# Performance work log

Measured on AMD Instinct MI355X. Metric: run time of the kernel, lower is better.

The kernel has to match this reference:

```python
import jax, jax.numpy as jnp
import numpy as np

B, C, EMB, W, H = 4, 128, 16, 64, 64


def setup_inputs() -> dict:
    key = jax.random.key(0)
    ks = jax.random.split(key, 8)
    return {
        "x": jax.random.normal(ks[0], (B, C, W, H), dtype=jnp.float32),
        "Wq": jax.random.normal(ks[1], (EMB, C), dtype=jnp.float32) * (1.0 / np.sqrt(C)),
        "bq": jax.random.normal(ks[2], (EMB,), dtype=jnp.float32) * 0.01,
        "Wk": jax.random.normal(ks[3], (EMB, C), dtype=jnp.float32) * (1.0 / np.sqrt(C)),
        "bk": jax.random.normal(ks[4], (EMB,), dtype=jnp.float32) * 0.01,
        "Wv": jax.random.normal(ks[5], (C, C), dtype=jnp.float32) * (1.0 / np.sqrt(C)),
        "bv": jax.random.normal(ks[6], (C,), dtype=jnp.float32) * 0.01,
        "gamma": jax.random.normal(ks[7], (1,), dtype=jnp.float32),
    }


def reference(x, Wq, bq, Wk, bk, Wv, bv, gamma):
    b, c, w, h = x.shape
    n = w * h
    xf = x.reshape(b, c, n)  # flatten spatial: [b, c, n]
    # 1x1 convs == per-pixel linear maps
    q = jnp.einsum('ec,bcn->bne', Wq, xf) + bq                # [b, n, emb]
    k = jnp.einsum('ec,bcn->ben', Wk, xf) + bk[:, None]       # [b, emb, n]
    energy = jnp.einsum('bne,bem->bnm', q, k)                 # [b, n, n] (unscaled)
    attn = jax.nn.softmax(energy, axis=-1)                    # softmax over keys m
    v = jnp.einsum('dc,bcn->bdn', Wv, xf) + bv[:, None]       # [b, c, n]
    # torch: out = bmm(V, attn^T) -> out[b,d,n] = sum_m V[b,d,m] * attn[b,n,m]
    out = jnp.einsum('bdm,bnm->bdn', v, attn)
    out = (gamma * out + xf).reshape(b, c, w, h)
    return out
```

## Files before the change

kernel.cpp:

```cpp
#include <hip/hip_runtime.h>


#define PEXP(s) exp2f(fmaf((s), 1.44269504f, -23.08312065f))

typedef __attribute__((ext_vector_type(8))) short bf16x8;
typedef __attribute__((ext_vector_type(4))) float f32x4;
typedef __attribute__((ext_vector_type(4))) int i32x4;

__device__ __forceinline__ bf16x8 asbf(i32x4 v) {
  return __builtin_bit_cast(bf16x8, v);
}
__device__ __forceinline__ int cvtpk(float lo, float hi) {
  int r;
  asm("v_cvt_pk_bf16_f32 %0, %1, %2" : "=v"(r) : "v"(lo), "v"(hi));
  return r;
}
__device__ __forceinline__ float lo16f(int u) {
  return __uint_as_float(((unsigned)u) << 16);
}
__device__ __forceinline__ float hi16f(int u) {
  return __uint_as_float(((unsigned)u) & 0xffff0000u);
}
__device__ __forceinline__ void async16(const void* g, void* l) {
  __builtin_amdgcn_global_load_lds(
      (const __attribute__((address_space(1))) void*)g,
      (__attribute__((address_space(3))) void*)l, 16, 0, 0);
}


__global__ __launch_bounds__(256, 2) void proj_kernel(
    const float* __restrict__ xg, const float* __restrict__ Wq,
    const float* __restrict__ bq, const float* __restrict__ Wk,
    const float* __restrict__ bk, const float* __restrict__ Wv,
    const float* __restrict__ bv, char* __restrict__ Qg,
    char* __restrict__ Kg, char* __restrict__ Vg) {
  __shared__ __align__(16) float xl[8192];
  __shared__ __align__(16) float wl[10240];
  const int bid = blockIdx.x;
  const int xcd = bid & 7, b = xcd >> 1, dh = xcd & 1, pt = bid >> 3;
  const int n0 = pt << 6;
  const int tid = threadIdx.x;

  const float* Wqk = dh ? Wk : Wq;
#pragma unroll
  for (int k = 0; k < 8; k++) {
    int idx = tid + k * 256;
    int cc = idx >> 4, p4 = (idx & 15) << 2;
    const float* src = xg + ((size_t)(b * 128 + cc)) * 4096 + n0 + p4;
    async16(src, (char*)xl + idx * 16);
  }
#pragma unroll
  for (int k = 0; k < 10; k++) {
    int j = tid + k * 256;
    int row = j >> 5, c4 = (j & 31) * 4;
    const float* src = (k < 8) ? (Wv + (size_t)(dh * 64 + row) * 128 + c4)
                               : (Wqk + (size_t)(row - 64) * 128 + c4);
    async16(src, (char*)wl + j * 16);
  }
  asm volatile("s_waitcnt vmcnt(0)" ::: "memory");
  __syncthreads();

  const int px = tid & 63, og = tid >> 6;

  float av[16];
#pragma unroll
  for (int i = 0; i < 16; i++) av[i] = 0.f;
  float aq[4] = {0.f, 0.f, 0.f, 0.f};

  for (int c0 = 0; c0 < 128; c0 += 4) {
    float x0 = xl[(c0 + 0) * 64 + px];
    float x1 = xl[(c0 + 1) * 64 + px];
    float x2 = xl[(c0 + 2) * 64 + px];
    float x3 = xl[(c0 + 3) * 64 + px];
#pragma unroll
    for (int r = 0; r < 16; r++) {
      const float* wr = &wl[(og * 16 + r) * 128 + c0];
      av[r] += wr[0] * x0 + wr[1] * x1 + wr[2] * x2 + wr[3] * x3;
    }
#pragma unroll
    for (int ee = 0; ee < 4; ee++) {
      const float* wr = &wl[(64 + og * 4 + ee) * 128 + c0];
      aq[ee] += wr[0] * x0 + wr[1] * x1 + wr[2] * x2 + wr[3] * x3;
    }
  }

  {
    const float* bqk = dh ? bk : bq;
    float v0 = aq[0] + bqk[og * 4 + 0], v1 = aq[1] + bqk[og * 4 + 1];
    float v2 = aq[2] + bqk[og * 4 + 2], v3 = aq[3] + bqk[og * 4 + 3];
    int h0 = cvtpk(v0, v1), h1 = cvtpk(v2, v3);
    float r0 = v0 - lo16f(h0), r1 = v1 - hi16f(h0);
    float r2 = v2 - lo16f(h1), r3 = v3 - hi16f(h1);
    int l0 = cvtpk(r0, r1), l1 = cvtpk(r2, r3);
    i32x4 ch = {h0, h1, l0, l1};
    char* QKg = dh ? Kg : Qg;
    *(i32x4*)(QKg + ((size_t)(b * 16384 + og * 4096 + n0 + px)) * 16) = ch;
  }

  const int d0 = dh * 64 + og * 16;
  __syncthreads();
#pragma unroll
  for (int r = 0; r < 16; r++) xl[(og * 16 + r) * 64 + px] = av[r] + bv[d0 + r];
  __syncthreads();

  char* vg_t = Vg + (size_t)b * 2097152 + (size_t)pt * 32768;
#pragma unroll
  for (int k = 0; k < 4; k++) {
    int id = tid + k * 256;
    int gs = id & 3, d1 = (id >> 2) & 63, kc = id >> 8;
    int d = dh * 64 + d1;
    int gg = gs ^ ((d >> 1) & 3);
    f32x4 v = *(const f32x4*)&xl[d1 * 64 + kc * 16 + gg * 4];
    int h0 = cvtpk(v[0], v[1]), h1 = cvtpk(v[2], v[3]);
    float r0 = v[0] - lo16f(h0), r1 = v[1] - hi16f(h0);
    float r2 = v[2] - lo16f(h1), r3 = v[3] - hi16f(h1);
    int l0 = cvtpk(r0, r1), l1 = cvtpk(r2, r3);
    i32x4 ch = {h0, h1, l0, l1};
    *(i32x4*)(vg_t + ((size_t)((kc * 128 + d) * 4 + gs)) * 16) = ch;
  }
}

#define COMPUTE(KF, V0, V1, V2, V3)                                            \
  {                                                                            \
    i32x4 k2 = {KF[2], KF[3], KF[0], KF[1]};                                   \
    __builtin_amdgcn_s_setprio(1);                                             \
    f32x4 s0 = __builtin_amdgcn_mfma_f32_16x16x32_bf16(asbf(KF), asbf(qf0),    \
                                                       zero4, 0, 0, 0);        \
    s0 = __builtin_amdgcn_mfma_f32_16x16x32_bf16(asbf(k2), asbf(qf0), s0, 0,   \
                                                 0, 0);                        \
    f32x4 s1 = __builtin_amdgcn_mfma_f32_16x16x32_bf16(asbf(KF), asbf(qf1),    \
                                                       zero4, 0, 0, 0);        \
    s1 = __builtin_amdgcn_mfma_f32_16x16x32_bf16(asbf(k2), asbf(qf1), s1, 0,   \
                                                 0, 0);                        \
    __builtin_amdgcn_s_setprio(0);                                             \
    bf16x8 a0, a1;                                                             \
    {                                                                          \
      float p0 = PEXP(s0[0]), p1 = PEXP(s0[1]), p2 = PEXP(s0[2]),              \
            p3 = PEXP(s0[3]);                                                  \
      lsum0 += (p0 + p1) + (p2 + p3);                                          \
      int h0 = cvtpk(p0, p1), h1 = cvtpk(p2, p3);                              \
      i32x4 A = {h0, h1, h0, h1};                                              \
      a0 = asbf(A);                                                            \
    }                                                                          \
    {                                                                          \
      float p0 = PEXP(s1[0]), p1 = PEXP(s1[1]), p2 = PEXP(s1[2]),              \
            p3 = PEXP(s1[3]);                                                  \
      lsum1 += (p0 + p1) + (p2 + p3);                                          \
      int h0 = cvtpk(p0, p1), h1 = cvtpk(p2, p3);                              \
      i32x4 A = {h0, h1, h0, h1};                                              \
      a1 = asbf(A);                                                            \
    }                                                                          \
    __builtin_amdgcn_s_setprio(1);                                             \
    acc[0][0] = __builtin_amdgcn_mfma_f32_16x16x32_bf16(a0, asbf(V0),          \
                                                        acc[0][0], 0, 0, 0);   \
    acc[0][1] = __builtin_amdgcn_mfma_f32_16x16x32_bf16(a0, asbf(V1),          \
                                                        acc[0][1], 0, 0, 0);   \
    acc[0][2] = __builtin_amdgcn_mfma_f32_16x16x32_bf16(a0, asbf(V2),          \
                                                        acc[0][2], 0, 0, 0);   \
    acc[0][3] = __builtin_amdgcn_mfma_f32_16x16x32_bf16(a0, asbf(V3),          \
                                                        acc[0][3], 0, 0, 0);   \
    acc[1][0] = __builtin_amdgcn_mfma_f32_16x16x32_bf16(a1, asbf(V0),          \
                                                        acc[1][0], 0, 0, 0);   \
    acc[1][1] = __builtin_amdgcn_mfma_f32_16x16x32_bf16(a1, asbf(V1),          \
                                                        acc[1][1], 0, 0, 0);   \
    acc[1][2] = __builtin_amdgcn_mfma_f32_16x16x32_bf16(a1, asbf(V2),          \
                                                        acc[1][2], 0, 0, 0);   \
    acc[1][3] = __builtin_amdgcn_mfma_f32_16x16x32_bf16(a1, asbf(V3),          \
                                                        acc[1][3], 0, 0, 0);   \
    __builtin_amdgcn_s_setprio(0);                                             \
  }

#define LOADSET(KF, V0, V1, V2, V3, tt)                                        \
  {                                                                            \
    const char* vp = vlane + (size_t)(tt)*32768;                               \
    V0 = *(const i32x4*)(vp);                                                  \
    V1 = *(const i32x4*)(vp + 1024);                                           \
    V2 = *(const i32x4*)(vp + 2048);                                           \
    V3 = *(const i32x4*)(vp + 3072);                                           \
    KF = *(const i32x4*)(kg_b + ((size_t)(g * 4096 + (tt)*64 + krow)) * 16);   \
  }

__global__ __launch_bounds__(512, 4) void flash_kernel(
    const char* __restrict__ Qg, const char* __restrict__ Kg,
    const char* __restrict__ Vg, const float* __restrict__ xg,
    const float* __restrict__ gammag, float* __restrict__ outg) {
  __shared__ float red_O[32 * 129];
  __shared__ float red_L[32];

  const int bid = blockIdx.x;
  const int xcd = bid & 7;
  const int b = xcd >> 1;
  const int nt = ((bid >> 3) << 1) | (xcd & 1);
  const int n0 = nt << 5;

  const int tid = threadIdx.x;
  const int l = tid & 63, w = tid >> 6;
  const int c = l & 15, g = l >> 4;
  const int kc = w & 3, dh = w >> 2;

  const char* kg_b = Kg + (size_t)b * 262144;
  const char* vg_b = Vg + (size_t)b * 2097152;
  const char* vlane =
      vg_b + ((size_t)(kc * 512 + dh * 256 + c * 4 + (g ^ ((c >> 1) & 3)))) * 16;
  const int krow = kc * 16 + c;

  const i32x4 qf0 =
      *(const i32x4*)(Qg + ((size_t)(b * 16384 + g * 4096 + n0 + c)) * 16);
  const i32x4 qf1 =
      *(const i32x4*)(Qg + ((size_t)(b * 16384 + g * 4096 + n0 + 16 + c)) * 16);

  const f32x4 zero4 = {0.f, 0.f, 0.f, 0.f};
  f32x4 acc[2][4];
#pragma unroll
  for (int qt = 0; qt < 2; qt++)
#pragma unroll
    for (int dt = 0; dt < 4; dt++) acc[qt][dt] = zero4;
  float lsum0 = 0.f, lsum1 = 0.f;

  i32x4 ka, va0, va1, va2, va3;
  i32x4 kb, vb0, vb1, vb2, vb3;
  LOADSET(ka, va0, va1, va2, va3, 0);
  LOADSET(kb, vb0, vb1, vb2, vb3, 1);

  for (int t = 0; t < 64; t += 2) {
    COMPUTE(ka, va0, va1, va2, va3);
    {
      int t2 = (t + 2 < 64) ? t + 2 : 63;
      LOADSET(ka, va0, va1, va2, va3, t2);
    }
    COMPUTE(kb, vb0, vb1, vb2, vb3);
    {
      int t3 = (t + 3 < 64) ? t + 3 : 63;
      LOADSET(kb, vb0, vb1, vb2, vb3, t3);
    }
  }

  for (int i = tid; i < 32 * 129; i += 512) red_O[i] = 0.f;
  if (tid < 32) red_L[tid] = 0.f;
  __syncthreads();

  {
    float s = lsum0;
    s += __shfl_xor(s, 16);
    s += __shfl_xor(s, 32);
    if (g == 0 && dh == 0) atomicAdd(&red_L[c], s);
    s = lsum1;
    s += __shfl_xor(s, 16);
    s += __shfl_xor(s, 32);
    if (g == 0 && dh == 0) atomicAdd(&red_L[16 + c], s);
  }
#pragma unroll
  for (int qt = 0; qt < 2; qt++) {
#pragma unroll
    for (int dt = 0; dt < 4; dt++) {
#pragma unroll
      for (int i = 0; i < 4; i++) {
        atomicAdd(&red_O[(qt * 16 + 4 * g + i) * 129 + dh * 64 + dt * 16 + c],
                  acc[qt][dt][i]);
      }
    }
  }
  __syncthreads();

  const float gam = gammag[0];
#pragma unroll
  for (int k = 0; k < 2; k++) {
    int id = tid + k * 512;
    int q4 = id & 7, d = id >> 3;
    int q0 = q4 * 4;
    size_t base = ((size_t)(b * 128 + d)) * 4096 + n0 + q0;
    f32x4 x4 = *(const f32x4*)(xg + base);
    f32x4 o;
#pragma unroll
    for (int j = 0; j < 4; j++)
      o[j] = gam * (red_O[(q0 + j) * 129 + d] / red_L[q0 + j]) + x4[j];
    *(f32x4*)(outg + base) = o;
  }
}

extern "C" void kernel_launch(void* const* d_in, const int* in_sizes, int n_in,
                              void* d_out, int out_size, void* d_ws, size_t ws_size,
                              hipStream_t stream) {
  (void)in_sizes; (void)n_in; (void)out_size; (void)ws_size;
  const float* x = (const float*)d_in[0];
  const float* Wq = (const float*)d_in[1];
  const float* bq = (const float*)d_in[2];
  const float* Wk = (const float*)d_in[3];
  const float* bk = (const float*)d_in[4];
  const float* Wv = (const float*)d_in[5];
  const float* bv = (const float*)d_in[6];
  const float* gamma = (const float*)d_in[7];
  float* out = (float*)d_out;

  char* Qg = (char*)d_ws;
  char* Kg = Qg + (1 << 20);
  char* Vg = Kg + (1 << 20);

  proj_kernel<<<512, 256, 0, stream>>>(x, Wq, bq, Wk, bk, Wv, bv, Qg, Kg, Vg);
  flash_kernel<<<512, 512, 0, stream>>>(Qg, Kg, Vg, x, gamma, out);
}
```

Before: 182.3 us.

## Use MFMA split-bf16 projections and widen flash tiles to 64 queries

The projection kernel moves from scalar FP32 FMAs to MFMA bf16 hi/lo split matmuls, with weights pre-packed into LDS. Each block now computes Q, K and V together for 64 pixels, and the V layout is simplified. The flash kernel now covers 64 queries per block, with warps splitting queries instead of output channels. Each warp loads all 128 V channels per key tile, so each K/V fetch is reused across twice as many queries. The cost is twice the accumulator registers, lower occupancy (launch bounds 2 instead of 4), and half as many blocks (256), which may underfill the GPU.

Result: faster. 175.2 us (-3.9%).

```diff
diff --git a/kernel.cpp b/kernel.cpp
--- a/kernel.cpp
+++ b/kernel.cpp
@@ -26,101 +26,117 @@
       (const __attribute__((address_space(1))) void*)g,
       (__attribute__((address_space(3))) void*)l, 16, 0, 0);
 }
-
-
-__global__ __launch_bounds__(256, 2) void proj_kernel(
+__device__ __forceinline__ i32x4 packhl(float v0, float v1, float v2, float v3) {
+  int h0 = cvtpk(v0, v1), h1 = cvtpk(v2, v3);
+  int l0 = cvtpk(v0 - lo16f(h0), v1 - hi16f(h0));
+  int l1 = cvtpk(v2 - lo16f(h1), v3 - hi16f(h1));
+  i32x4 r = {h0, h1, l0, l1};
+  return r;
+}
+
+
+__global__ __launch_bounds__(256, 1) void proj_kernel(
     const float* __restrict__ xg, const float* __restrict__ Wq,
     const float* __restrict__ bq, const float* __restrict__ Wk,
     const float* __restrict__ bk, const float* __restrict__ Wv,
     const float* __restrict__ bv, char* __restrict__ Qg,
     char* __restrict__ Kg, char* __restrict__ Vg) {
   __shared__ __align__(16) float xl[8192];
-  __shared__ __align__(16) float wl[10240];
+  __shared__ __align__(16) char wl[81920];
   const int bid = blockIdx.x;
-  const int xcd = bid & 7, b = xcd >> 1, dh = xcd & 1, pt = bid >> 3;
-  const int n0 = pt << 6;
+  const int xcd = bid & 7, b = xcd >> 1;
+  const int Pg = ((bid >> 3) << 1) | (xcd & 1);
+  const int n0 = Pg << 6;
   const int tid = threadIdx.x;
 
-  const float* Wqk = dh ? Wk : Wq;
 #pragma unroll
   for (int k = 0; k < 8; k++) {
     int idx = tid + k * 256;
     int cc = idx >> 4, p4 = (idx & 15) << 2;
-    const float* src = xg + ((size_t)(b * 128 + cc)) * 4096 + n0 + p4;
-    async16(src, (char*)xl + idx * 16);
-  }
-#pragma unroll
-  for (int k = 0; k < 10; k++) {
-    int j = tid + k * 256;
-    int row = j >> 5, c4 = (j & 31) * 4;
-    const float* src = (k < 8) ? (Wv + (size_t)(dh * 64 + row) * 128 + c4)
-                               : (Wqk + (size_t)(row - 64) * 128 + c4);
-    async16(src, (char*)wl + j * 16);
+    async16(xg + ((size_t)(b * 128 + cc)) * 4096 + n0 + p4,
+            (char*)xl + idx * 16);
+  }
+#pragma unroll
+  for (int k = 0; k < 20; k++) {
+    int wid = tid + k * 256;
+    int dd = wid & 15, g = (wid >> 4) & 3, m = (wid >> 6) & 7, r = wid >> 9;
+    const float* row = (r < 8) ? (Wv + (size_t)(r * 16 + dd) * 128)
+                               : ((r == 8) ? (Wq + (size_t)dd * 128)
+                                           : (Wk + (size_t)dd * 128));
+    f32x4 v = *(const f32x4*)(row + m * 16 + g * 4);
+    *(i32x4*)(wl + (size_t)wid * 16) = packhl(v[0], v[1], v[2], v[3]);
   }
   asm volatile("s_waitcnt vmcnt(0)" ::: "memory");
   __syncthreads();
 
-  const int px = tid & 63, og = tid >> 6;
-
-  float av[16];
-#pragma unroll
-  for (int i = 0; i < 16; i++) av[i] = 0.f;
-  float aq[4] = {0.f, 0.f, 0.f, 0.f};
-
-  for (int c0 = 0; c0 < 128; c0 += 4) {
-    float x0 = xl[(c0 + 0) * 64 + px];
-    float x1 = xl[(c0 + 1) * 64 + px];
-    float x2 = xl[(c0 + 2) * 64 + px];
-    float x3 = xl[(c0 + 3) * 64 + px];
-#pragma unroll
-    for (int r = 0; r < 16; r++) {
-      const float* wr = &wl[(og * 16 + r) * 128 + c0];
-      av[r] += wr[0] * x0 + wr[1] * x1 + wr[2] * x2 + wr[3] * x3;
+  const int l = tid & 63, w = tid >> 6;
+  const int p = l & 15, g = l >> 4;
+  const int P = Pg * 4 + w;
+  const int pxl = w * 16 + p;
+
+  float bvv[8];
+#pragma unroll
+  for (int r = 0; r < 8; r++) bvv[r] = bv[r * 16 + p];
+  float bq4[4], bk4[4];
+#pragma unroll
+  for (int i = 0; i < 4; i++) {
+    bq4[i] = bq[4 * g + i];
+    bk4[i] = bk[4 * g + i];
+  }
+
+  const f32x4 zero4 = {0.f, 0.f, 0.f, 0.f};
+  f32x4 acc[10];
+#pragma unroll
+  for (int r = 0; r < 10; r++) acc[r] = zero4;
+
+#pragma unroll
+  for (int m = 0; m < 8; m++) {
+    float x0 = xl[(16 * m + 4 * g + 0) * 64 + pxl];
+    float x1 = xl[(16 * m + 4 * g + 1) * 64 + pxl];
+    float x2 = xl[(16 * m + 4 * g + 2) * 64 + pxl];
+    float x3 = xl[(16 * m + 4 * g + 3) * 64 + pxl];
+    i32x4 xm = packhl(x0, x1, x2, x3);
+    i32x4 xs = {xm[2], xm[3], xm[0], xm[1]};
+#pragma unroll
+    for (int r = 0; r < 10; r++) {
+      i32x4 wm = *(const i32x4*)(wl + (size_t)((r * 8 + m) * 64 + l) * 16);
+      if (r < 8) {
+        acc[r] = __builtin_amdgcn_mfma_f32_16x16x32_bf16(asbf(xm), asbf(wm),
+                                                         acc[r], 0, 0, 0);
+        acc[r] = __builtin_amdgcn_mfma_f32_16x16x32_bf16(asbf(xs), asbf(wm),
+                                                         acc[r], 0, 0, 0);
+      } else {
+        acc[r] = __builtin_amdgcn_mfma_f32_16x16x32_bf16(asbf(wm), asbf(xm),
+                                                         acc[r], 0, 0, 0);
+        acc[r] = __builtin_amdgcn_mfma_f32_16x16x32_bf16(asbf(wm), asbf(xs),
+                                                         acc[r], 0, 0, 0);
+      }
     }
-#pragma unroll
-    for (int ee = 0; ee < 4; ee++) {
-      const float* wr = &wl[(64 + og * 4 + ee) * 128 + c0];
-      aq[ee] += wr[0] * x0 + wr[1] * x1 + wr[2] * x2 + wr[3] * x3;
-    }
-  }
-
+  }
+
+  const int t = P >> 2, kc = P & 3;
+  char* vg_t = Vg + (size_t)b * 2097152 + (size_t)t * 32768;
+#pragma unroll
+  for (int r = 0; r < 8; r++) {
+    float v0 = acc[r][0] + bvv[r], v1 = acc[r][1] + bvv[r];
+    float v2 = acc[r][2] + bvv[r], v3 = acc[r][3] + bvv[r];
+    int d = r * 16 + p;
+    *(i32x4*)(vg_t + ((size_t)((kc * 4 + g) * 128 + d)) * 16) =
+        packhl(v0, v1, v2, v3);
+  }
   {
-    const float* bqk = dh ? bk : bq;
-    float v0 = aq[0] + bqk[og * 4 + 0], v1 = aq[1] + bqk[og * 4 + 1];
-    float v2 = aq[2] + bqk[og * 4 + 2], v3 = aq[3] + bqk[og * 4 + 3];
-    int h0 = cvtpk(v0, v1), h1 = cvtpk(v2, v3);
-    float r0 = v0 - lo16f(h0), r1 = v1 - hi16f(h0);
-    float r2 = v2 - lo16f(h1), r3 = v3 - hi16f(h1);
-    int l0 = cvtpk(r0, r1), l1 = cvtpk(r2, r3);
-    i32x4 ch = {h0, h1, l0, l1};
-    char* QKg = dh ? Kg : Qg;
-    *(i32x4*)(QKg + ((size_t)(b * 16384 + og * 4096 + n0 + px)) * 16) = ch;
-  }
-
-  const int d0 = dh * 64 + og * 16;
-  __syncthreads();
-#pragma unroll
-  for (int r = 0; r < 16; r++) xl[(og * 16 + r) * 64 + px] = av[r] + bv[d0 + r];
-  __syncthreads();
-
-  char* vg_t = Vg + (size_t)b * 2097152 + (size_t)pt * 32768;
-#pragma unroll
-  for (int k = 0; k < 4; k++) {
-    int id = tid + k * 256;
-    int gs = id & 3, d1 = (id >> 2) & 63, kc = id >> 8;
-    int d = dh * 64 + d1;
-    int gg = gs ^ ((d >> 1) & 3);
-    f32x4 v = *(const f32x4*)&xl[d1 * 64 + kc * 16 + gg * 4];
-    int h0 = cvtpk(v[0], v[1]), h1 = cvtpk(v[2], v[3]);
-    float r0 = v[0] - lo16f(h0), r1 = v[1] - hi16f(h0);
-    float r2 = v[2] - lo16f(h1), r3 = v[3] - hi16f(h1);
-    int l0 = cvtpk(r0, r1), l1 = cvtpk(r2, r3);
-    i32x4 ch = {h0, h1, l0, l1};
-    *(i32x4*)(vg_t + ((size_t)((kc * 128 + d) * 4 + gs)) * 16) = ch;
-  }
-}
-
-#define COMPUTE(KF, V0, V1, V2, V3)                                            \
+    float v0 = acc[8][0] + bq4[0], v1 = acc[8][1] + bq4[1];
+    float v2 = acc[8][2] + bq4[2], v3 = acc[8][3] + bq4[3];
+    *(i32x4*)(Qg + ((size_t)(b * 16384 + g * 4096 + P * 16 + p)) * 16) =
+        packhl(v0, v1, v2, v3);
+    v0 = acc[9][0] + bk4[0]; v1 = acc[9][1] + bk4[1];
+    v2 = acc[9][2] + bk4[2]; v3 = acc[9][3] + bk4[3];
+    *(i32x4*)(Kg + ((size_t)(b * 16384 + g * 4096 + P * 16 + p)) * 16) =
+        packhl(v0, v1, v2, v3);
+  }
+}
+
+#define COMPUTE(KF, V0, V1, V2, V3, V4, V5, V6, V7)                            \
   {                                                                            \
     i32x4 k2 = {KF[2], KF[3], KF[0], KF[1]};                                   \
     __builtin_amdgcn_s_setprio(1);                                             \
@@ -151,122 +167,124 @@
       a1 = asbf(A);                                                            \
     }                                                                          \
     __builtin_amdgcn_s_setprio(1);                                             \
-    acc[0][0] = __builtin_amdgcn_mfma_f32_16x16x32_bf16(a0, asbf(V0),          \
-                                                        acc[0][0], 0, 0, 0);   \
-    acc[0][1] = __builtin_amdgcn_mfma_f32_16x16x32_bf16(a0, asbf(V1),          \
-                                                        acc[0][1], 0, 0, 0);   \
-    acc[0][2] = __builtin_amdgcn_mfma_f32_16x16x32_bf16(a0, asbf(V2),          \
-                                                        acc[0][2], 0, 0, 0);   \
-    acc[0][3] = __builtin_amdgcn_mfma_f32_16x16x32_bf16(a0, asbf(V3),          \
-                                                        acc[0][3], 0, 0, 0);   \
-    acc[1][0] = __builtin_amdgcn_mfma_f32_16x16x32_bf16(a1, asbf(V0),          \
-                                                        acc[1][0], 0, 0, 0);   \
-    acc[1][1] = __builtin_amdgcn_mfma_f32_16x16x32_bf16(a1, asbf(V1),          \
-                                                        acc[1][1], 0, 0, 0);   \
-    acc[1][2] = __builtin_amdgcn_mfma_f32_16x16x32_bf16(a1, asbf(V2),          \
-                                                        acc[1][2], 0, 0, 0);   \
-    acc[1][3] = __builtin_amdgcn_mfma_f32_16x16x32_bf16(a1, asbf(V3),          \
-                                                        acc[1][3], 0, 0, 0);   \
+    acc0[0] = __builtin_amdgcn_mfma_f32_16x16x32_bf16(a0, asbf(V0), acc0[0], 0, 0, 0); \
+    acc0[1] = __builtin_amdgcn_mfma_f32_16x16x32_bf16(a0, asbf(V1), acc0[1], 0, 0, 0); \
+    acc0[2] = __builtin_amdgcn_mfma_f32_16x16x32_bf16(a0, asbf(V2), acc0[2], 0, 0, 0); \
+    acc0[3] = __builtin_amdgcn_mfma_f32_16x16x32_bf16(a0, asbf(V3), acc0[3], 0, 0, 0); \
+    acc0[4] = __builtin_amdgcn_mfma_f32_16x16x32_bf16(a0, asbf(V4), acc0[4], 0, 0, 0); \
+    acc0[5] = __builtin_amdgcn_mfma_f32_16x16x32_bf16(a0, asbf(V5), acc0[5], 0, 0, 0); \
+    acc0[6] = __builtin_amdgcn_mfma_f32_16x16x32_bf16(a0, asbf(V6), acc0[6], 0, 0, 0); \
+    acc0[7] = __builtin_amdgcn_mfma_f32_16x16x32_bf16(a0, asbf(V7), acc0[7], 0, 0, 0); \
+    acc1[0] = __builtin_amdgcn_mfma_f32_16x16x32_bf16(a1, asbf(V0), acc1[0], 0, 0, 0); \
+    acc1[1] = __builtin_amdgcn_mfma_f32_16x16x32_bf16(a1, asbf(V1), acc1[1], 0, 0, 0); \
+    acc1[2] = __builtin_amdgcn_mfma_f32_16x16x32_bf16(a1, asbf(V2), acc1[2], 0, 0, 0); \
+    acc1[3] = __builtin_amdgcn_mfma_f32_16x16x32_bf16(a1, asbf(V3), acc1[3], 0, 0, 0); \
+    acc1[4] = __builtin_amdgcn_mfma_f32_16x16x32_bf16(a1, asbf(V4), acc1[4], 0, 0, 0); \
+    acc1[5] = __builtin_amdgcn_mfma_f32_16x16x32_bf16(a1, asbf(V5), acc1[5], 0, 0, 0); \
+    acc1[6] = __builtin_amdgcn_mfma_f32_16x16x32_bf16(a1, asbf(V6), acc1[6], 0, 0, 0); \
+    acc1[7] = __builtin_amdgcn_mfma_f32_16x16x32_bf16(a1, asbf(V7), acc1[7], 0, 0, 0); \
     __builtin_amdgcn_s_setprio(0);                                             \
   }
 
-#define LOADSET(KF, V0, V1, V2, V3, tt)                                        \
+#define LOADSET(KF, V0, V1, V2, V3, V4, V5, V6, V7, tt)                        \
   {                                                                            \
-    const char* vp = vlane + (size_t)(tt)*32768;                               \
-    V0 = *(const i32x4*)(vp);                                                  \
-    V1 = *(const i32x4*)(vp + 1024);                                           \
-    V2 = *(const i32x4*)(vp + 2048);                                           \
-    V3 = *(const i32x4*)(vp + 3072);                                           \
-    KF = *(const i32x4*)(kg_b + ((size_t)(g * 4096 + (tt)*64 + krow)) * 16);   \
-  }
-
-__global__ __launch_bounds__(512, 4) void flash_kernel(
+    unsigned vo = voff + (unsigned)(tt)*32768u;                                \
+    V0 = *(const i32x4*)(vg_b + vo);                                           \
+    V1 = *(const i32x4*)(vg_b + vo + 256);                                     \
+    V2 = *(const i32x4*)(vg_b + vo + 512);                                     \
+    V3 = *(const i32x4*)(vg_b + vo + 768);                                     \
+    V4 = *(const i32x4*)(vg_b + vo + 1024);                                    \
+    V5 = *(const i32x4*)(vg_b + vo + 1280);                                    \
+    V6 = *(const i32x4*)(vg_b + vo + 1536);                                    \
+    V7 = *(const i32x4*)(vg_b + vo + 1792);                                    \
+    KF = *(const i32x4*)(kg_b + koff + (unsigned)(tt)*1024u);                  \
+  }
+
+__global__ __launch_bounds__(512, 2) void flash_kernel(
     const char* __restrict__ Qg, const char* __restrict__ Kg,
     const char* __restrict__ Vg, const float* __restrict__ xg,
     const float* __restrict__ gammag, float* __restrict__ outg) {
-  __shared__ float red_O[32 * 129];
-  __shared__ float red_L[32];
+  __shared__ float red_O[64 * 129];
+  __shared__ float red_L[64];
 
   const int bid = blockIdx.x;
   const int xcd = bid & 7;
   const int b = xcd >> 1;
   const int nt = ((bid >> 3) << 1) | (xcd & 1);
-  const int n0 = nt << 5;
+  const int n0 = nt << 6;
 
   const int tid = threadIdx.x;
   const int l = tid & 63, w = tid >> 6;
   const int c = l & 15, g = l >> 4;
-  const int kc = w & 3, dh = w >> 2;
+  const int kc = w & 3, qh = w >> 2;
 
   const char* kg_b = Kg + (size_t)b * 262144;
   const char* vg_b = Vg + (size_t)b * 2097152;
-  const char* vlane =
-      vg_b + ((size_t)(kc * 512 + dh * 256 + c * 4 + (g ^ ((c >> 1) & 3)))) * 16;
-  const int krow = kc * 16 + c;
-
-  const i32x4 qf0 =
-      *(const i32x4*)(Qg + ((size_t)(b * 16384 + g * 4096 + n0 + c)) * 16);
-  const i32x4 qf1 =
-      *(const i32x4*)(Qg + ((size_t)(b * 16384 + g * 4096 + n0 + 16 + c)) * 16);
+  const unsigned voff = (unsigned)(((kc * 4 + g) * 128 + c) * 16);
+  const unsigned koff = (unsigned)((g * 4096 + kc * 16 + c) * 16);
+
+  const i32x4 qf0 = *(const i32x4*)(
+      Qg + ((size_t)(b * 16384 + g * 4096 + n0 + qh * 32 + c)) * 16);
+  const i32x4 qf1 = *(const i32x4*)(
+      Qg + ((size_t)(b * 16384 + g * 4096 + n0 + qh * 32 + 16 + c)) * 16);
 
   const f32x4 zero4 = {0.f, 0.f, 0.f, 0.f};
-  f32x4 acc[2][4];
-#pragma unroll
-  for (int qt = 0; qt < 2; qt++)
-#pragma unroll
-    for (int dt = 0; dt < 4; dt++) acc[qt][dt] = zero4;
+  f32x4 acc0[8], acc1[8];
+#pragma unroll
+  for (int dt = 0; dt < 8; dt++) {
+    acc0[dt] = zero4;
+    acc1[dt] = zero4;
+  }
   float lsum0 = 0.f, lsum1 = 0.f;
 
-  i32x4 ka, va0, va1, va2, va3;
-  i32x4 kb, vb0, vb1, vb2, vb3;
-  LOADSET(ka, va0, va1, va2, va3, 0);
-  LOADSET(kb, vb0, vb1, vb2, vb3, 1);
+  i32x4 ka, va0, va1, va2, va3, va4, va5, va6, va7;
+  i32x4 kb, vb0, vb1, vb2, vb3, vb4, vb5, vb6, vb7;
+  LOADSET(ka, va0, va1, va2, va3, va4, va5, va6, va7, 0);
+  LOADSET(kb, vb0, vb1, vb2, vb3, vb4, vb5, vb6, vb7, 1);
 
   for (int t = 0; t < 64; t += 2) {
-    COMPUTE(ka, va0, va1, va2, va3);
+    COMPUTE(ka, va0, va1, va2, va3, va4, va5, va6, va7);
     {
       int t2 = (t + 2 < 64) ? t + 2 : 63;
-      LOADSET(ka, va0, va1, va2, va3, t2);
+      LOADSET(ka, va0, va1, va2, va3, va4, va5, va6, va7, t2);
     }
-    COMPUTE(kb, vb0, vb1, vb2, vb3);
+    COMPUTE(kb, vb0, vb1, vb2, vb3, vb4, vb5, vb6, vb7);
     {
       int t3 = (t + 3 < 64) ? t + 3 : 63;
-      LOADSET(kb, vb0, vb1, vb2, vb3, t3);
+      LOADSET(kb, vb0, vb1, vb2, vb3, vb4, vb5, vb6, vb7, t3);
     }
   }
 
-  for (int i = tid; i < 32 * 129; i += 512) red_O[i] = 0.f;
-  if (tid < 32) red_L[tid] = 0.f;
+  for (int i = tid; i < 64 * 129; i += 512) red_O[i] = 0.f;
+  if (tid < 64) red_L[tid] = 0.f;
   __syncthreads();
 
   {
     float s = lsum0;
     s += __shfl_xor(s, 16);
     s += __shfl_xor(s, 32);
-    if (g == 0 && dh == 0) atomicAdd(&red_L[c], s);
+    if (g == 0) atomicAdd(&red_L[qh * 32 + c], s);
     s = lsum1;
     s += __shfl_xor(s, 16);
     s += __shfl_xor(s, 32);
-    if (g == 0 && dh == 0) atomicAdd(&red_L[16 + c], s);
-  }
-#pragma unroll
-  for (int qt = 0; qt < 2; qt++) {
-#pragma unroll
-    for (int dt = 0; dt < 4; dt++) {
-#pragma unroll
-      for (int i = 0; i < 4; i++) {
-        atomicAdd(&red_O[(qt * 16 + 4 * g + i) * 129 + dh * 64 + dt * 16 + c],
-                  acc[qt][dt][i]);
-      }
+    if (g == 0) atomicAdd(&red_L[qh * 32 + 16 + c], s);
+  }
+#pragma unroll
+  for (int dt = 0; dt < 8; dt++) {
+#pragma unroll
+    for (int i = 0; i < 4; i++) {
+      atomicAdd(&red_O[(qh * 32 + 4 * g + i) * 129 + dt * 16 + c], acc0[dt][i]);
+      atomicAdd(&red_O[(qh * 32 + 16 + 4 * g + i) * 129 + dt * 16 + c],
+                acc1[dt][i]);
     }
   }
   __syncthreads();
 
   const float gam = gammag[0];
 #pragma unroll
-  for (int k = 0; k < 2; k++) {
+  for (int k = 0; k < 4; k++) {
     int id = tid + k * 512;
-    int q4 = id & 7, d = id >> 3;
+    int q4 = id & 15, d = id >> 4;
     int q0 = q4 * 4;
     size_t base = ((size_t)(b * 128 + d)) * 4096 + n0 + q0;
     f32x4 x4 = *(const f32x4*)(xg + base);
@@ -296,6 +314,6 @@
   char* Kg = Qg + (1 << 20);
   char* Vg = Kg + (1 << 20);
 
-  proj_kernel<<<512, 256, 0, stream>>>(x, Wq, bq, Wk, bk, Wv, bv, Qg, Kg, Vg);
-  flash_kernel<<<512, 512, 0, stream>>>(Qg, Kg, Vg, x, gamma, out);
-}
+  proj_kernel<<<256, 256, 0, stream>>>(x, Wq, bq, Wk, bk, Wv, bv, Qg, Kg, Vg);
+  flash_kernel<<<256, 512, 0, stream>>>(Qg, Kg, Vg, x, gamma, out);
+}
```
